# Kernel tuning notes

Measured on AMD Instinct MI355X. Metric: run time of the kernel, lower is better.

The kernel has to match this reference:

```python
import jax, jax.numpy as jnp
import numpy as np

EPS_DIST = 1e-8
EPS_BN = 1e-5


def _bn_relu(x, g, b):
    # training-mode BatchNorm1d over (batch, spatial) per channel, then ReLU
    mean = jnp.mean(x, axis=(0, 2), keepdims=True)
    var = jnp.mean((x - mean) ** 2, axis=(0, 2), keepdims=True)
    xhat = (x - mean) * jax.lax.rsqrt(var + EPS_BN)
    return jax.nn.relu(xhat * g[None, :, None] + b[None, :, None])


def setup_inputs() -> dict:
    key = jax.random.key(0)
    ks = jax.random.split(key, 8)
    B, N, M, C1, C2 = 8, 16384, 4096, 64, 256
    return {
        "p1": jax.random.normal(ks[0], (B, N, 3), jnp.float32),
        "p2": jax.random.normal(ks[1], (B, M, 3), jnp.float32),
        "f1": jax.random.normal(ks[2], (B, C1, N), jnp.float32),
        "f2": jax.random.normal(ks[3], (B, C2, M), jnp.float32),
        "idx": jax.random.randint(ks[4], (B, N, 3), 0, M, jnp.int64),
        "W1": jax.random.normal(ks[5], (256, C1 + C2), jnp.float32) * 0.05,
        "g1": jnp.ones((256,), jnp.float32),
        "b1": jnp.zeros((256,), jnp.float32),
        "W2": jax.random.normal(ks[6], (256, 256), jnp.float32) * 0.05,
        "g2": jnp.ones((256,), jnp.float32),
        "b2": jnp.zeros((256,), jnp.float32),
    }


def reference(p1, p2, f1, f2, idx, W1, g1, b1, W2, g2, b2):
    B = p1.shape[0]
    b_ix = jnp.arange(B)[:, None, None]  # batch index for gathers
    # --- three_interpolation: inverse-squared-distance weighted 3-NN interp ---
    nbr_xyz = p2[b_ix, idx]                     # [B, N, 3, 3]
    d2 = jnp.sum((p1[:, :, None, :] - nbr_xyz) ** 2, axis=-1)  # [B, N, 3]
    recip = 1.0 / (d2 + EPS_DIST)
    weight = recip / jnp.sum(recip, axis=-1, keepdims=True)    # [B, N, 3]
    f2_nbr = jnp.swapaxes(f2, 1, 2)[b_ix, idx]  # [B, N, 3, C2]
    interp = jnp.einsum("bnkc,bnk->bcn", f2_nbr, weight)       # [B, C2, N]
    # --- concat + two 1x1 conv + BN + ReLU blocks ---
    x = jnp.concatenate((f1, interp), axis=1)   # [B, C1+C2, N]
    x = _bn_relu(jnp.einsum("oi,bin->bon", W1, x), g1, b1)
    x = _bn_relu(jnp.einsum("oi,bin->bon", W2, x), g2, b2)
    return x
```

## Files before the change

### kernel.cpp

```cpp
#include <hip/hip_runtime.h>
#include <hip/hip_bf16.h>

#define BB 8
#define NN 16384
#define MM 4096
#define C1 64
#define C2 256
#define K1 320
#define CO 256
#define MTOT (BB * NN)

#define STATS_OFF 0
#define FLAG_OFF  8192
#define W1B_OFF   16384
#define W2B_OFF   180224
#define F2T_OFF   327680
#define XT_OFF    (327680 + 16777216)
#define H2_OFF    (327680 + 16777216 + 83886080)


typedef short v8s __attribute__((ext_vector_type(8)));
typedef float v4f __attribute__((ext_vector_type(4)));

__device__ __forceinline__ float bf2f(unsigned short u) {
    unsigned v = ((unsigned)u) << 16;
    float f;
    __builtin_memcpy(&f, &v, 4);
    return f;
}
__device__ __forceinline__ unsigned short f2bf(float f) {
    unsigned u;
    __builtin_memcpy(&u, &f, 4);
    unsigned r = u + 0x7fffu + ((u >> 16) & 1u);
    return (unsigned short)(r >> 16);
}
__device__ __forceinline__ void gload16(const unsigned short* g, unsigned short* l) {
    __builtin_amdgcn_global_load_lds((const __attribute__((address_space(1))) unsigned int*)g,
                                     (__attribute__((address_space(3))) unsigned int*)l, 16, 0, 0);
}

__global__ void k_pre(const void* idx_raw, int* flag64, float* stats,
                      const float* __restrict__ W1, unsigned short* __restrict__ W1b,
                      const float* __restrict__ W2, unsigned short* __restrict__ W2b,
                      const float* __restrict__ f2, unsigned short* __restrict__ f2t,
                      const float* __restrict__ f1, unsigned short* __restrict__ xT) {
    __shared__ float tile[64][33];
    int blk = blockIdx.x;
    int t = threadIdx.x;
    if (blk < 320) {
        int e = blk * 256 + t;
        int row = e / K1, col = e - row * K1;
        W1b[row * K1 + (col ^ ((row & 7) << 3))] = f2bf(W1[e]);
    } else if (blk < 576) {
        int e = (blk - 320) * 256 + t;
        int row = e >> 8, col = e & 255;
        W2b[row * CO + (col ^ ((row & 7) << 3))] = f2bf(W2[e]);
    } else if (blk == 576) {
        for (int i = t; i < 8 * 256; i += 256) stats[i] = 0.f;
        if (t == 0) {
            const int* a = (const int*)idx_raw;
            int all0 = 1;
            for (int j = 1; j < 64; j += 2) all0 &= (a[j] == 0);
            *flag64 = all0;
        }
    } else if (blk < 577 + 4096) {
        int i = blk - 577;
        int m0 = (i & 127) * 32;
        int c0 = ((i >> 7) & 3) * 64;
        int b = i >> 9;
        int lm = t & 31, lc = t >> 5;
        const float* src = f2 + ((size_t)b * C2 + c0) * MM + m0;
#pragma unroll
        for (int j = 0; j < 8; ++j)
            tile[lc + 8 * j][lm] = src[(size_t)(lc + 8 * j) * MM + lm];
        __syncthreads();
        int m = t >> 3, c8 = (t & 7) * 8;
        unsigned short tmp[8];
#pragma unroll
        for (int k = 0; k < 8; ++k) tmp[k] = f2bf(tile[c8 + k][m]);
        uint4 v;
        v.x = (unsigned)tmp[0] | ((unsigned)tmp[1] << 16);
        v.y = (unsigned)tmp[2] | ((unsigned)tmp[3] << 16);
        v.z = (unsigned)tmp[4] | ((unsigned)tmp[5] << 16);
        v.w = (unsigned)tmp[6] | ((unsigned)tmp[7] << 16);
        *(uint4*)&f2t[((size_t)b * MM + m0 + m) * C2 + c0 + c8] = v;
    } else {
        int i = blk - 4673;
        int n0 = (i & 511) * 32;
        int b = i >> 9;
        int lm = t & 31, lc = t >> 5;
        const float* src = f1 + ((size_t)b * C1) * NN + n0;
#pragma unroll
        for (int j = 0; j < 8; ++j)
            tile[lc + 8 * j][lm] = src[(size_t)(lc + 8 * j) * NN + lm];
        __syncthreads();
        int m = t >> 3, c8 = (t & 7) * 8;
        unsigned short tmp[8];
#pragma unroll
        for (int k = 0; k < 8; ++k) tmp[k] = f2bf(tile[c8 + k][m]);
        uint4 v;
        v.x = (unsigned)tmp[0] | ((unsigned)tmp[1] << 16);
        v.y = (unsigned)tmp[2] | ((unsigned)tmp[3] << 16);
        v.z = (unsigned)tmp[4] | ((unsigned)tmp[5] << 16);
        v.w = (unsigned)tmp[6] | ((unsigned)tmp[7] << 16);
        *(uint4*)&xT[((size_t)b * NN + n0 + m) * K1 + (c8 ^ ((m & 7) * 8))] = v;
    }
}

__global__ void k_interp(const float* __restrict__ p1, const float* __restrict__ p2,
                         const void* __restrict__ idxv, const int* __restrict__ flag64,
                         const unsigned short* __restrict__ f2t,
                         unsigned short* __restrict__ xT) {
    int t = threadIdx.x;
    int p = t >> 5, lane = t & 31;
    size_t pt = (size_t)blockIdx.x * 8 + p;
    int b = (int)(pt >> 14);
    int m0, m1, m2;
    if (*flag64) {
        const long long* id = (const long long*)idxv;
        m0 = (int)id[pt * 3 + 0]; m1 = (int)id[pt * 3 + 1]; m2 = (int)id[pt * 3 + 2];
    } else {
        const int* id = (const int*)idxv;
        m0 = id[pt * 3 + 0]; m1 = id[pt * 3 + 1]; m2 = id[pt * 3 + 2];
    }
    float qx = p1[pt * 3 + 0], qy = p1[pt * 3 + 1], qz = p1[pt * 3 + 2];
    const float* pb = p2 + (size_t)b * MM * 3;
    float dx, dy, dz;
    dx = qx - pb[m0 * 3 + 0]; dy = qy - pb[m0 * 3 + 1]; dz = qz - pb[m0 * 3 + 2];
    float d0 = dx * dx + dy * dy + dz * dz;
    dx = qx - pb[m1 * 3 + 0]; dy = qy - pb[m1 * 3 + 1]; dz = qz - pb[m1 * 3 + 2];
    float d1 = dx * dx + dy * dy + dz * dz;
    dx = qx - pb[m2 * 3 + 0]; dy = qy - pb[m2 * 3 + 1]; dz = qz - pb[m2 * 3 + 2];
    float d2v = dx * dx + dy * dy + dz * dz;
    float r0 = 1.f / (d0 + 1e-8f), r1 = 1.f / (d1 + 1e-8f), r2 = 1.f / (d2v + 1e-8f);
    float inv = 1.f / (r0 + r1 + r2);
    float w0 = r0 * inv, w1 = r1 * inv, w2 = r2 * inv;

    const unsigned short* fb = f2t + (size_t)b * MM * C2;
    int c0 = lane * 8;
    uint4 va = *(const uint4*)(fb + (size_t)m0 * C2 + c0);
    uint4 vb = *(const uint4*)(fb + (size_t)m1 * C2 + c0);
    uint4 vc = *(const uint4*)(fb + (size_t)m2 * C2 + c0);

    float r[8];
    {
        const unsigned av[4] = {va.x, va.y, va.z, va.w};
        const unsigned bv[4] = {vb.x, vb.y, vb.z, vb.w};
        const unsigned cv[4] = {vc.x, vc.y, vc.z, vc.w};
#pragma unroll
        for (int q = 0; q < 4; ++q) {
            r[2 * q + 0] = w0 * bf2f((unsigned short)(av[q] & 0xffff))
                         + w1 * bf2f((unsigned short)(bv[q] & 0xffff))
                         + w2 * bf2f((unsigned short)(cv[q] & 0xffff));
            r[2 * q + 1] = w0 * bf2f((unsigned short)(av[q] >> 16))
                         + w1 * bf2f((unsigned short)(bv[q] >> 16))
                         + w2 * bf2f((unsigned short)(cv[q] >> 16));
        }
    }
    uint4 outv;
    outv.x = (unsigned)f2bf(r[0]) | ((unsigned)f2bf(r[1]) << 16);
    outv.y = (unsigned)f2bf(r[2]) | ((unsigned)f2bf(r[3]) << 16);
    outv.z = (unsigned)f2bf(r[4]) | ((unsigned)f2bf(r[5]) << 16);
    outv.w = (unsigned)f2bf(r[6]) | ((unsigned)f2bf(r[7]) << 16);
    *(uint4*)(xT + pt * K1 + ((C1 + c0) ^ (((int)pt & 7) * 8))) = outv;
}

#define TM 128
#define TN 128
#define TK 64
__launch_bounds__(256)
__global__ void k_gemm1(const unsigned short* __restrict__ xT,
                        const unsigned short* __restrict__ W1b,
                        unsigned short* __restrict__ h1,
                        float* __restrict__ sum1, float* __restrict__ ssq1) {
    __shared__ unsigned short smem[2][TM * TK + TN * TK];
    const int t = threadIdx.x;
    const int lane = t & 63, w = t >> 6;
    const int wm = w >> 1, wc = w & 1;
    const long rbase = (long)blockIdx.y * TM;
    const int cb = blockIdx.x * TN;

    v4f acc[4][4];
#pragma unroll
    for (int r = 0; r < 4; ++r)
#pragma unroll
        for (int c = 0; c < 4; ++c) acc[r][c] = (v4f)(0.f);

    const int srow = w * 32 + (lane >> 3);
    const int sch = (lane & 7) * 8;
    const unsigned short* Ag = xT + (rbase + srow) * K1 + sch;
    const unsigned short* Bg = W1b + (size_t)(cb + srow) * K1 + sch;

    const int ln = lane & 15, q = lane >> 4;
    const int xs = (ln & 7) * 8;

#pragma unroll
    for (int j = 0; j < 4; ++j) {
        gload16(Ag + (size_t)(j * 8) * K1, smem[0] + (w * 32 + j * 8) * TK);
        gload16(Bg + (size_t)(j * 8) * K1, smem[0] + TM * TK + (w * 32 + j * 8) * TK);
    }

    for (int k0 = 0; k0 < K1; k0 += TK) {
        const int p = (k0 >> 6) & 1;
        if (k0 + TK < K1) {
#pragma unroll
            for (int j = 0; j < 4; ++j) {
                gload16(Ag + (size_t)(j * 8) * K1 + k0 + TK, smem[p ^ 1] + (w * 32 + j * 8) * TK);
                gload16(Bg + (size_t)(j * 8) * K1 + k0 + TK, smem[p ^ 1] + TM * TK + (w * 32 + j * 8) * TK);
            }
            asm volatile("s_waitcnt vmcnt(8)" ::: "memory");
        } else {
            asm volatile("s_waitcnt vmcnt(0)" ::: "memory");
        }
        asm volatile("s_barrier" ::: "memory");
        __builtin_amdgcn_sched_barrier(0);
        const unsigned short* ApL = smem[p] + (wm * 64 + ln) * TK;
        const unsigned short* BpL = smem[p] + TM * TK + (wc * 64 + ln) * TK;
#pragma unroll
        for (int ks = 0; ks < 2; ++ks) {
            const int off = (q * 8 + ks * 32) ^ xs;
            v8s af[4], bg[4];
#pragma unroll
            for (int r = 0; r < 4; ++r) af[r] = *(const v8s*)(ApL + r * 16 * TK + off);
#pragma unroll
            for (int c = 0; c < 4; ++c) bg[c] = *(const v8s*)(BpL + c * 16 * TK + off);
#pragma unroll
            for (int r = 0; r < 4; ++r)
#pragma unroll
                for (int c = 0; c < 4; ++c)
                    acc[r][c] = __builtin_amdgcn_mfma_f32_16x16x32_bf16(af[r], bg[c], acc[r][c], 0, 0, 0);
        }
        __builtin_amdgcn_sched_barrier(0);
        if (k0 + TK < K1) asm volatile("s_barrier" ::: "memory");
    }
    __syncthreads();

    unsigned short* ep = (unsigned short*)smem;
#pragma unroll
    for (int c = 0; c < 4; ++c) {
        int col = wc * 64 + c * 16 + ln;
        int cc = col >> 3, ci = col & 7;
        float s = 0.f, sq = 0.f;
#pragma unroll
        for (int r = 0; r < 4; ++r)
#pragma unroll
            for (int i = 0; i < 4; ++i) {
                int row = wm * 64 + r * 16 + q * 4 + i;
                float v = acc[r][c][i];
                ep[row * 128 + 8 * (cc ^ (row & 15)) + ci] = f2bf(v);
                s += v; sq += v * v;
            }
        s += __shfl_xor(s, 16); sq += __shfl_xor(sq, 16);
        s += __shfl_xor(s, 32); sq += __shfl_xor(sq, 32);
        if (lane < 16) {
            atomicAdd(&sum1[cb + col], s);
            atomicAdd(&ssq1[cb + col], sq);
        }
    }
    __syncthreads();
    {
        int rr = t >> 4, cc2 = t & 15;
#pragma unroll
        for (int j = 0; j < 8; ++j) {
            int row = rr + 16 * j;
            uint4 v = *(const uint4*)&ep[row * 128 + 8 * (cc2 ^ (row & 15))];
            *(uint4*)&h1[(size_t)(rbase + row) * CO + cb + cc2 * 8] = v;
        }
    }
}

__launch_bounds__(256)
__global__ void k_gemm2(const unsigned short* __restrict__ h1,
                        const unsigned short* __restrict__ W2b,
                        const float* __restrict__ sum1, const float* __restrict__ ssq1,
                        const float* __restrict__ g1, const float* __restrict__ b1,
                        unsigned short* __restrict__ h2,
                        float* __restrict__ sum2, float* __restrict__ ssq2) {
    __shared__ unsigned short smem[2][TM * TK + TN * TK];
    __shared__ float sc1[CO], sh1[CO];
    const int t = threadIdx.x;
    const int lane = t & 63, w = t >> 6;
    const int wm = w >> 1, wc = w & 1;
    const long rbase = (long)blockIdx.y * TM;
    const int cb = blockIdx.x * TN;

    {
        const float invn = 1.f / (float)MTOT;
        float m = sum1[t] * invn;
        float v = ssq1[t] * invn - m * m;
        float s = g1[t] * rsqrtf(v + 1e-5f);
        sc1[t] = s;
        sh1[t] = b1[t] - m * s;
    }
    __syncthreads();

    v4f acc[4][4];
#pragma unroll
    for (int r = 0; r < 4; ++r)
#pragma unroll
        for (int c = 0; c < 4; ++c) acc[r][c] = (v4f)(0.f);

    const int srow = w * 32 + (lane >> 3);
    const int sch = (lane & 7) * 8;
    const unsigned short* Ag = h1 + (rbase + srow) * CO + sch;
    const unsigned short* Bg = W2b + (size_t)(cb + srow) * CO + sch;
    const int awz = srow * TK + (sch ^ ((srow & 7) * 8));

    const int ln = lane & 15, q = lane >> 4;
    const int xs = (ln & 7) * 8;

#define CONV_STORE(AV, KOFF, BASE)                                                     \
    do {                                                                               \
        float4 sca = *(const float4*)(sc1 + (KOFF) + sch);                             \
        float4 scb = *(const float4*)(sc1 + (KOFF) + sch + 4);                         \
        float4 sha = *(const float4*)(sh1 + (KOFF) + sch);                             \
        float4 shb = *(const float4*)(sh1 + (KOFF) + sch + 4);                         \
        _Pragma("unroll")                                                              \
        for (int j = 0; j < 4; ++j) {                                                  \
            uint4 av = (AV)[j];                                                        \
            float y0 = fmaxf(bf2f((unsigned short)(av.x & 0xffff)) * sca.x + sha.x, 0.f); \
            float y1 = fmaxf(bf2f((unsigned short)(av.x >> 16)) * sca.y + sha.y, 0.f); \
            float y2 = fmaxf(bf2f((unsigned short)(av.y & 0xffff)) * sca.z + sha.z, 0.f); \
            float y3 = fmaxf(bf2f((unsigned short)(av.y >> 16)) * sca.w + sha.w, 0.f); \
            float y4 = fmaxf(bf2f((unsigned short)(av.z & 0xffff)) * scb.x + shb.x, 0.f); \
            float y5 = fmaxf(bf2f((unsigned short)(av.z >> 16)) * scb.y + shb.y, 0.f); \
            float y6 = fmaxf(bf2f((unsigned short)(av.w & 0xffff)) * scb.z + shb.z, 0.f); \
            float y7 = fmaxf(bf2f((unsigned short)(av.w >> 16)) * scb.w + shb.w, 0.f); \
            uint4 ov;                                                                  \
            asm("v_cvt_pk_bf16_f32 %0, %1, %2" : "=v"(ov.x) : "v"(y0), "v"(y1));       \
            asm("v_cvt_pk_bf16_f32 %0, %1, %2" : "=v"(ov.y) : "v"(y2), "v"(y3));       \
            asm("v_cvt_pk_bf16_f32 %0, %1, %2" : "=v"(ov.z) : "v"(y4), "v"(y5));       \
            asm("v_cvt_pk_bf16_f32 %0, %1, %2" : "=v"(ov.w) : "v"(y6), "v"(y7));       \
            *(uint4*)((BASE) + awz + (j * 8) * TK) = ov;                               \
        }                                                                              \
    } while (0)

    uint4 avc[4], avn[4];
#pragma unroll
    for (int j = 0; j < 4; ++j)
        gload16(Bg + (size_t)(j * 8) * CO, smem[0] + TM * TK + (w * 32 + j * 8) * TK);
#pragma unroll
    for (int j = 0; j < 4; ++j) avc[j] = *(const uint4*)(Ag + (size_t)(j * 8) * CO);
#pragma unroll
    for (int j = 0; j < 4; ++j) avn[j] = *(const uint4*)(Ag + (size_t)(j * 8) * CO + TK);
    CONV_STORE(avc, 0, smem[0]);
    __syncthreads();

#pragma unroll
    for (int kk = 0; kk < 4; ++kk) {
        const int p = kk & 1;
        if (kk < 3) {
#pragma unroll
            for (int j = 0; j < 4; ++j)
                gload16(Bg + (size_t)(j * 8) * CO + (kk + 1) * TK,
                        smem[p ^ 1] + TM * TK + (w * 32 + j * 8) * TK);
            CONV_STORE(avn, (kk + 1) * TK, smem[p ^ 1]);
        }
        if (kk < 2) {
#pragma unroll
            for (int j = 0; j < 4; ++j)
                avn[j] = *(const uint4*)(Ag + (size_t)(j * 8) * CO + (kk + 2) * TK);
        }
        const unsigned short* ApL = smem[p] + (wm * 64 + ln) * TK;
        const unsigned short* BpL = smem[p] + TM * TK + (wc * 64 + ln) * TK;
#pragma unroll
        for (int ks = 0; ks < 2; ++ks) {
            const int off = (q * 8 + ks * 32) ^ xs;
            v8s af[4], bg4[4];
#pragma unroll
            for (int r = 0; r < 4; ++r) af[r] = *(const v8s*)(ApL + r * 16 * TK + off);
#pragma unroll
            for (int c = 0; c < 4; ++c) bg4[c] = *(const v8s*)(BpL + c * 16 * TK + off);
#pragma unroll
            for (int r = 0; r < 4; ++r)
#pragma unroll
                for (int c = 0; c < 4; ++c)
                    acc[r][c] = __builtin_amdgcn_mfma_f32_16x16x32_bf16(af[r], bg4[c], acc[r][c], 0, 0, 0);
        }
        __syncthreads();
    }
#undef CONV_STORE

    unsigned short* ep = (unsigned short*)smem;
    const int b = (int)(rbase >> 14);
    const int nb = (int)(rbase & (NN - 1));
#pragma unroll
    for (int c = 0; c < 4; ++c) {
        int ol = wc * 64 + c * 16 + ln;
        float s = 0.f, sq = 0.f;
#pragma unroll
        for (int r = 0; r < 4; ++r)
#pragma unroll
            for (int i = 0; i < 4; ++i) {
                int row = wm * 64 + r * 16 + q * 4 + i;
                int rc = row >> 3, ri = row & 7;
                float v = acc[r][c][i];
                ep[ol * 128 + 8 * (rc ^ (ol & 15)) + ri] = f2bf(v);
                s += v; sq += v * v;
            }
        s += __shfl_xor(s, 16); sq += __shfl_xor(sq, 16);
        s += __shfl_xor(s, 32); sq += __shfl_xor(sq, 32);
        if (lane < 16) {
            atomicAdd(&sum2[cb + ol], s);
            atomicAdd(&ssq2[cb + ol], sq);
        }
    }
    __syncthreads();
    {
        int oo = t >> 4, nc = t & 15;
#pragma unroll
        for (int j = 0; j < 8; ++j) {
            int ol = oo + 16 * j;
            uint4 v = *(const uint4*)&ep[ol * 128 + 8 * (nc ^ (ol & 15))];
            *(uint4*)&h2[(((size_t)(b * CO + cb + ol)) << 14) + nb + nc * 8] = v;
        }
    }
}

__global__ void k_apply(const unsigned short* __restrict__ h2,
                        const float* __restrict__ sum2, const float* __restrict__ ssq2,
                        const float* __restrict__ g2, const float* __restrict__ b2,
                        float* __restrict__ out) {
    __shared__ float ss[2];
    int o = (blockIdx.x >> 3) & 255;
    if (threadIdx.x == 0) {
        const float invn = 1.f / (float)MTOT;
        float m = sum2[o] * invn;
        float v = ssq2[o] * invn - m * m;
        float s = g2[o] * rsqrtf(v + 1e-5f);
        ss[0] = s;
        ss[1] = b2[o] - m * s;
    }
    __syncthreads();
    float s = ss[0], d = ss[1];
    size_t i = ((size_t)blockIdx.x * 256 + threadIdx.x) * 8;
    uint4 hv = *(const uint4*)(h2 + i);
    float4 v0, v1;
    v0.x = fmaxf(bf2f((unsigned short)(hv.x & 0xffff)) * s + d, 0.f);
    v0.y = fmaxf(bf2f((unsigned short)(hv.x >> 16)) * s + d, 0.f);
    v0.z = fmaxf(bf2f((unsigned short)(hv.y & 0xffff)) * s + d, 0.f);
    v0.w = fmaxf(bf2f((unsigned short)(hv.y >> 16)) * s + d, 0.f);
    v1.x = fmaxf(bf2f((unsigned short)(hv.z & 0xffff)) * s + d, 0.f);
    v1.y = fmaxf(bf2f((unsigned short)(hv.z >> 16)) * s + d, 0.f);
    v1.z = fmaxf(bf2f((unsigned short)(hv.w & 0xffff)) * s + d, 0.f);
    v1.w = fmaxf(bf2f((unsigned short)(hv.w >> 16)) * s + d, 0.f);
    *(float4*)&out[i] = v0;
    *(float4*)&out[i + 4] = v1;
}

extern "C" void kernel_launch(void* const* d_in, const int* in_sizes, int n_in,
                              void* d_out, int out_size, void* d_ws, size_t ws_size,
                              hipStream_t stream) {
    const float* p1 = (const float*)d_in[0];
    const float* p2 = (const float*)d_in[1];
    const float* f1 = (const float*)d_in[2];
    const float* f2 = (const float*)d_in[3];
    const void*  idx = d_in[4];
    const float* W1 = (const float*)d_in[5];
    const float* g1 = (const float*)d_in[6];
    const float* b1 = (const float*)d_in[7];
    const float* W2 = (const float*)d_in[8];
    const float* g2 = (const float*)d_in[9];
    const float* b2 = (const float*)d_in[10];
    float* out = (float*)d_out;

    char* ws = (char*)d_ws;
    float* stats = (float*)(ws + STATS_OFF);
    float* sum1 = stats + 0;     float* ssq1 = stats + 256;
    float* sum2 = stats + 1024;  float* ssq2 = stats + 1280;
    int* flag64 = (int*)(ws + FLAG_OFF);
    unsigned short* W1b = (unsigned short*)(ws + W1B_OFF);
    unsigned short* W2b = (unsigned short*)(ws + W2B_OFF);
    unsigned short* f2t = (unsigned short*)(ws + F2T_OFF);
    unsigned short* xT  = (unsigned short*)(ws + XT_OFF);
    unsigned short* h2  = (unsigned short*)(ws + H2_OFF);

    unsigned short* h1 = (unsigned short*)d_out;

    k_pre<<<577 + 4096 + 4096, 256, 0, stream>>>(idx, flag64, stats, W1, W1b, W2, W2b,
                                                 f2, f2t, f1, xT);
    k_interp<<<MTOT / 8, 256, 0, stream>>>(p1, p2, idx, flag64, f2t, xT);
    k_gemm1<<<dim3(CO / TN, MTOT / TM), 256, 0, stream>>>(xT, W1b, h1, sum1, ssq1);
    k_gemm2<<<dim3(CO / TN, MTOT / TM), 256, 0, stream>>>(h1, W2b, sum1, ssq1, g1, b1, h2, sum2, ssq2);
    k_apply<<<(int)((size_t)out_size / 2048), 256, 0, stream>>>(h2, sum2, ssq2, g2, b2, out);
}
```

Baseline: 399.3 us.

## Load pre-swizzled h1 tiles directly to LDS and apply BN1 at fragment read

The first GEMM's epilogue now writes h1 with an XOR chunk swizzle, so the second GEMM can copy A tiles straight from global memory into LDS with async gload16, the same way it already loads the W2 tiles. The BN1 scale/shift and ReLU are applied when each MFMA A fragment is read from LDS, instead of in a register round-trip before the LDS store. The k-loop uses explicit vmcnt waits and raw barriers to double-buffer both operands. The trade-off is that the BN/ReLU conversion is now repeated for each column-warp sharing the same A rows, adding VALU work inside the MFMA loop.

```diff
diff --git a/kernel.cpp b/kernel.cpp
--- a/kernel.cpp
+++ b/kernel.cpp
@@ -264,7 +264,8 @@
         for (int j = 0; j < 8; ++j) {
             int row = rr + 16 * j;
             uint4 v = *(const uint4*)&ep[row * 128 + 8 * (cc2 ^ (row & 15))];
-            *(uint4*)&h1[(size_t)(rbase + row) * CO + cb + cc2 * 8] = v;
+            int swch = (cc2 & 8) | ((cc2 ^ row) & 7);
+            *(uint4*)&h1[(size_t)(rbase + row) * CO + cb + swch * 8] = v;
         }
     }
 }
@@ -304,71 +305,59 @@
     const int sch = (lane & 7) * 8;
     const unsigned short* Ag = h1 + (rbase + srow) * CO + sch;
     const unsigned short* Bg = W2b + (size_t)(cb + srow) * CO + sch;
-    const int awz = srow * TK + (sch ^ ((srow & 7) * 8));
 
     const int ln = lane & 15, q = lane >> 4;
     const int xs = (ln & 7) * 8;
 
-#define CONV_STORE(AV, KOFF, BASE)                                                     \
-    do {                                                                               \
-        float4 sca = *(const float4*)(sc1 + (KOFF) + sch);                             \
-        float4 scb = *(const float4*)(sc1 + (KOFF) + sch + 4);                         \
-        float4 sha = *(const float4*)(sh1 + (KOFF) + sch);                             \
-        float4 shb = *(const float4*)(sh1 + (KOFF) + sch + 4);                         \
-        _Pragma("unroll")                                                              \
-        for (int j = 0; j < 4; ++j) {                                                  \
-            uint4 av = (AV)[j];                                                        \
-            float y0 = fmaxf(bf2f((unsigned short)(av.x & 0xffff)) * sca.x + sha.x, 0.f); \
-            float y1 = fmaxf(bf2f((unsigned short)(av.x >> 16)) * sca.y + sha.y, 0.f); \
-            float y2 = fmaxf(bf2f((unsigned short)(av.y & 0xffff)) * sca.z + sha.z, 0.f); \
-            float y3 = fmaxf(bf2f((unsigned short)(av.y >> 16)) * sca.w + sha.w, 0.f); \
-            float y4 = fmaxf(bf2f((unsigned short)(av.z & 0xffff)) * scb.x + shb.x, 0.f); \
-            float y5 = fmaxf(bf2f((unsigned short)(av.z >> 16)) * scb.y + shb.y, 0.f); \
-            float y6 = fmaxf(bf2f((unsigned short)(av.w & 0xffff)) * scb.z + shb.z, 0.f); \
-            float y7 = fmaxf(bf2f((unsigned short)(av.w >> 16)) * scb.w + shb.w, 0.f); \
-            uint4 ov;                                                                  \
-            asm("v_cvt_pk_bf16_f32 %0, %1, %2" : "=v"(ov.x) : "v"(y0), "v"(y1));       \
-            asm("v_cvt_pk_bf16_f32 %0, %1, %2" : "=v"(ov.y) : "v"(y2), "v"(y3));       \
-            asm("v_cvt_pk_bf16_f32 %0, %1, %2" : "=v"(ov.z) : "v"(y4), "v"(y5));       \
-            asm("v_cvt_pk_bf16_f32 %0, %1, %2" : "=v"(ov.w) : "v"(y6), "v"(y7));       \
-            *(uint4*)((BASE) + awz + (j * 8) * TK) = ov;                               \
-        }                                                                              \
-    } while (0)
-
-    uint4 avc[4], avn[4];
-#pragma unroll
-    for (int j = 0; j < 4; ++j)
+#pragma unroll
+    for (int j = 0; j < 4; ++j) {
+        gload16(Ag + (size_t)(j * 8) * CO, smem[0] + (w * 32 + j * 8) * TK);
         gload16(Bg + (size_t)(j * 8) * CO, smem[0] + TM * TK + (w * 32 + j * 8) * TK);
-#pragma unroll
-    for (int j = 0; j < 4; ++j) avc[j] = *(const uint4*)(Ag + (size_t)(j * 8) * CO);
-#pragma unroll
-    for (int j = 0; j < 4; ++j) avn[j] = *(const uint4*)(Ag + (size_t)(j * 8) * CO + TK);
-    CONV_STORE(avc, 0, smem[0]);
-    __syncthreads();
-
-#pragma unroll
-    for (int kk = 0; kk < 4; ++kk) {
-        const int p = kk & 1;
-        if (kk < 3) {
-#pragma unroll
-            for (int j = 0; j < 4; ++j)
-                gload16(Bg + (size_t)(j * 8) * CO + (kk + 1) * TK,
-                        smem[p ^ 1] + TM * TK + (w * 32 + j * 8) * TK);
-            CONV_STORE(avn, (kk + 1) * TK, smem[p ^ 1]);
-        }
-        if (kk < 2) {
-#pragma unroll
-            for (int j = 0; j < 4; ++j)
-                avn[j] = *(const uint4*)(Ag + (size_t)(j * 8) * CO + (kk + 2) * TK);
-        }
+    }
+
+    for (int k0 = 0; k0 < CO; k0 += TK) {
+        const int p = (k0 >> 6) & 1;
+        if (k0 + TK < CO) {
+#pragma unroll
+            for (int j = 0; j < 4; ++j) {
+                gload16(Ag + (size_t)(j * 8) * CO + k0 + TK, smem[p ^ 1] + (w * 32 + j * 8) * TK);
+                gload16(Bg + (size_t)(j * 8) * CO + k0 + TK, smem[p ^ 1] + TM * TK + (w * 32 + j * 8) * TK);
+            }
+            asm volatile("s_waitcnt vmcnt(8)" ::: "memory");
+        } else {
+            asm volatile("s_waitcnt vmcnt(0)" ::: "memory");
+        }
+        asm volatile("s_barrier" ::: "memory");
+        __builtin_amdgcn_sched_barrier(0);
         const unsigned short* ApL = smem[p] + (wm * 64 + ln) * TK;
         const unsigned short* BpL = smem[p] + TM * TK + (wc * 64 + ln) * TK;
 #pragma unroll
         for (int ks = 0; ks < 2; ++ks) {
             const int off = (q * 8 + ks * 32) ^ xs;
+            const int koff = k0 + ks * 32 + q * 8;
+            float4 sca = *(const float4*)(sc1 + koff);
+            float4 scb = *(const float4*)(sc1 + koff + 4);
+            float4 sha = *(const float4*)(sh1 + koff);
+            float4 shb = *(const float4*)(sh1 + koff + 4);
             v8s af[4], bg4[4];
 #pragma unroll
-            for (int r = 0; r < 4; ++r) af[r] = *(const v8s*)(ApL + r * 16 * TK + off);
+            for (int r = 0; r < 4; ++r) {
+                uint4 raw = *(const uint4*)(ApL + r * 16 * TK + off);
+                float y0 = fmaxf(bf2f((unsigned short)(raw.x & 0xffff)) * sca.x + sha.x, 0.f);
+                float y1 = fmaxf(bf2f((unsigned short)(raw.x >> 16)) * sca.y + sha.y, 0.f);
+                float y2 = fmaxf(bf2f((unsigned short)(raw.y & 0xffff)) * sca.z + sha.z, 0.f);
+                float y3 = fmaxf(bf2f((unsigned short)(raw.y >> 16)) * sca.w + sha.w, 0.f);
+                float y4 = fmaxf(bf2f((unsigned short)(raw.z & 0xffff)) * scb.x + shb.x, 0.f);
+                float y5 = fmaxf(bf2f((unsigned short)(raw.z >> 16)) * scb.y + shb.y, 0.f);
+                float y6 = fmaxf(bf2f((unsigned short)(raw.w & 0xffff)) * scb.z + shb.z, 0.f);
+                float y7 = fmaxf(bf2f((unsigned short)(raw.w >> 16)) * scb.w + shb.w, 0.f);
+                uint4 cv;
+                asm("v_cvt_pk_bf16_f32 %0, %1, %2" : "=v"(cv.x) : "v"(y0), "v"(y1));
+                asm("v_cvt_pk_bf16_f32 %0, %1, %2" : "=v"(cv.y) : "v"(y2), "v"(y3));
+                asm("v_cvt_pk_bf16_f32 %0, %1, %2" : "=v"(cv.z) : "v"(y4), "v"(y5));
+                asm("v_cvt_pk_bf16_f32 %0, %1, %2" : "=v"(cv.w) : "v"(y6), "v"(y7));
+                __builtin_memcpy(&af[r], &cv, 16);
+            }
 #pragma unroll
             for (int c = 0; c < 4; ++c) bg4[c] = *(const v8s*)(BpL + c * 16 * TK + off);
 #pragma unroll
@@ -377,9 +366,10 @@
                 for (int c = 0; c < 4; ++c)
                     acc[r][c] = __builtin_amdgcn_mfma_f32_16x16x32_bf16(af[r], bg4[c], acc[r][c], 0, 0, 0);
         }
-        __syncthreads();
-    }
-#undef CONV_STORE
+        __builtin_amdgcn_sched_barrier(0);
+        if (k0 + TK < CO) asm volatile("s_barrier" ::: "memory");
+    }
+    __syncthreads();
 
     unsigned short* ep = (unsigned short*)smem;
     const int b = (int)(rbase >> 14);
```

Measured after the change: 399.9 us. Within noise of the previous version (+0.2%).
